# Performance work log

Measured on AMD Instinct MI355X. Metric: run time of the kernel, lower is better.

The kernel has to match this reference:

```python
import jax, jax.numpy as jnp
import numpy as np

B, L, D, H = 2, 4096, 512, 8
HD = D // H
SCALE = 1.0 / (D / H) ** 0.5


def setup_inputs() -> dict:
    key = jax.random.key(0)
    ks = jax.random.split(key, 12)
    s = 0.02
    inp = {
        "q": jax.random.normal(ks[0], (B, L, D), jnp.float32),
        "k": jax.random.normal(ks[1], (B, L, D), jnp.float32),
        "v": jax.random.normal(ks[2], (B, L, D), jnp.float32),
        # causal mask, True = keep (masked_fill where mask == False)
        "mask": jnp.tril(jnp.ones((L, L), bool))[None, None, :, :],
        "Wq": jax.random.normal(ks[3], (D, D), jnp.float32) * s,
        "bq": jnp.zeros((D,), jnp.float32),
        "Wk": jax.random.normal(ks[4], (D, D), jnp.float32) * s,
        "bk": jnp.zeros((D,), jnp.float32),
        "Wv": jax.random.normal(ks[5], (D, D), jnp.float32) * s,
        "bv": jnp.zeros((D,), jnp.float32),
        "Wo": jax.random.normal(ks[6], (D, D), jnp.float32) * s,
        "bo": jnp.zeros((D,), jnp.float32),
    }
    return inp


def _split_heads(x):
    # [B, L, D] -> [B, H, L, HD]
    b, l, d = x.shape
    return x.reshape(b, l, H, HD).transpose(0, 2, 1, 3)


def reference(q, k, v, mask, Wq, bq, Wk, bk, Wv, bv, Wo, bo):
    # Dropout is inference-mode (identity), matching module.eval().
    qh = _split_heads(q @ Wq.T + bq)          # [B,H,L,HD]
    kh = _split_heads(k @ Wk.T + bk)          # [B,H,L,HD]
    vh = _split_heads(v @ Wv.T + bv)          # [B,H,L,HD]
    scores = jnp.einsum("bhqd,bhkd->bhqk", qh, kh) * SCALE
    scores = jnp.where(mask, scores, -jnp.inf)
    attn = jax.nn.softmax(scores, axis=-1)
    out = jnp.einsum("bhqk,bhkd->bhqd", attn, vh)  # [B,H,L,HD]
    out = out.transpose(0, 2, 1, 3).reshape(q.shape[0], q.shape[1], D)
    return out @ Wo.T + bo
```

## Files before the change

### kernel.cpp

```cpp
#include <hip/hip_runtime.h>

typedef __bf16 bf16;
typedef __bf16 bf16x4 __attribute__((ext_vector_type(4)));
typedef __bf16 bf16x8 __attribute__((ext_vector_type(8)));
typedef float  f32x4  __attribute__((ext_vector_type(4)));
typedef float  f32x16 __attribute__((ext_vector_type(16)));
typedef unsigned int u32x2 __attribute__((ext_vector_type(2)));
typedef unsigned int u32x4 __attribute__((ext_vector_type(4)));

#define NB   2
#define NL   4096
#define ND   512
#define NH   8
#define NHD  64

static __device__ __forceinline__ void g2l16(const bf16* g, bf16* l) {
    __builtin_amdgcn_global_load_lds(
        (const __attribute__((address_space(1))) unsigned int*)g,
        (__attribute__((address_space(3))) unsigned int*)l, 16, 0, 0);
}

__global__ __launch_bounds__(256) void cvt_all(
    const float* __restrict__ q, const float* __restrict__ k, const float* __restrict__ v,
    const float* __restrict__ Wq, const float* __restrict__ Wk,
    const float* __restrict__ Wv, const float* __restrict__ Wo,
    bf16* __restrict__ qb, bf16* __restrict__ kb, bf16* __restrict__ vb,
    bf16* __restrict__ wqb, bf16* __restrict__ wkb,
    bf16* __restrict__ wvb, bf16* __restrict__ wob)
{
    const int z = blockIdx.z;
    const float* src; bf16* dst; int n4;
    switch (z) {
        case 0: src = q;  dst = qb;  n4 = NB * NL * ND / 4; break;
        case 1: src = k;  dst = kb;  n4 = NB * NL * ND / 4; break;
        case 2: src = v;  dst = vb;  n4 = NB * NL * ND / 4; break;
        case 3: src = Wq; dst = wqb; n4 = ND * ND / 4; break;
        case 4: src = Wk; dst = wkb; n4 = ND * ND / 4; break;
        case 5: src = Wv; dst = wvb; n4 = ND * ND / 4; break;
        default: src = Wo; dst = wob; n4 = ND * ND / 4; break;
    }
    for (int i = blockIdx.x * 256 + threadIdx.x; i < n4; i += gridDim.x * 256) {
        const f32x4 a = *(const f32x4*)(src + (size_t)i * 4);
        bf16x4 o;
        #pragma unroll
        for (int j = 0; j < 4; ++j) o[j] = (bf16)a[j];
        *(bf16x4*)(dst + (size_t)i * 4) = o;
    }
}

__global__ __launch_bounds__(256) void proj_qkv(
    const bf16* __restrict__ qb, const bf16* __restrict__ kb, const bf16* __restrict__ vb,
    const bf16* __restrict__ wq, const bf16* __restrict__ wk, const bf16* __restrict__ wv,
    const float* __restrict__ biasq, const float* __restrict__ biask, const float* __restrict__ biasv,
    bf16* __restrict__ qh, bf16* __restrict__ kh, bf16* __restrict__ vt)
{
    const int z = blockIdx.z;
    const bf16* X     = (z == 0) ? qb : (z == 1) ? kb : vb;
    const bf16* W     = (z == 0) ? wq : (z == 1) ? wk : wv;
    const float* bias = (z == 0) ? biasq : (z == 1) ? biask : biasv;

    const int m0 = blockIdx.y * 128;
    const int n0 = blockIdx.x * 128;

    __shared__ bf16 As[2][128 * 32];
    __shared__ bf16 Bs[2][128 * 32];

    const int t    = threadIdx.x;
    const int lane = t & 63;
    const int wm   = (t >> 7) & 1;
    const int wn   = (t >> 6) & 1;
    const int quad = lane >> 4;
    const int l16  = lane & 15;

    auto stage = [&](int k0, int buf) {
        #pragma unroll
        for (int p = 0; p < 2; ++p) {
            const int id = p * 256 + t;
            const int r = id >> 2, s = id & 3;
            const int c = (s ^ (r & 3)) * 8;
            g2l16(X + (size_t)(m0 + r) * ND + k0 + c, As[buf] + id * 8);
            g2l16(W + (size_t)(n0 + r) * ND + k0 + c, Bs[buf] + id * 8);
        }
    };

    f32x4 acc[4][4] = {};
    stage(0, 0);

    for (int it = 0; it < 16; ++it) {
        __syncthreads();
        if (it + 1 < 16) stage((it + 1) * 32, (it + 1) & 1);

        const bf16* as = As[it & 1];
        const bf16* bs = Bs[it & 1];
        bf16x8 aF[4], bF[4];
        #pragma unroll
        for (int i = 0; i < 4; ++i) {
            const int ra = wm * 64 + i * 16 + l16;
            const int rb = wn * 64 + i * 16 + l16;
            aF[i] = *(const bf16x8*)(as + ra * 32 + (quad ^ (ra & 3)) * 8);
            bF[i] = *(const bf16x8*)(bs + rb * 32 + (quad ^ (rb & 3)) * 8);
        }
        #pragma unroll
        for (int mt = 0; mt < 4; ++mt)
            #pragma unroll
            for (int nt = 0; nt < 4; ++nt)
                acc[mt][nt] = __builtin_amdgcn_mfma_f32_16x16x32_bf16(
                    aF[mt], bF[nt], acc[mt][nt], 0, 0, 0);
    }

    const float oscale = (z == 0) ? 0.125f : (z == 1) ? 1.4426950408889634f : 1.0f;
    #pragma unroll
    for (int nt = 0; nt < 4; ++nt) {
        const int col = n0 + wn * 64 + nt * 16 + l16;
        const float bb = bias[col];
        const int h = col >> 6, hd = col & 63;
        #pragma unroll
        for (int mt = 0; mt < 4; ++mt) {
            const int row0 = m0 + wm * 64 + mt * 16 + quad * 4;
            const int b = row0 >> 12;
            const int l = row0 & 4095;
            if (z == 2) {
                bf16x4 val;
                #pragma unroll
                for (int r = 0; r < 4; ++r) val[r] = (bf16)(acc[mt][nt][r] + bb);
                *(bf16x4*)(vt + ((size_t)(b * NH + h) * NHD + hd) * NL + l) = val;
            } else {
                bf16* dst = (z == 0) ? qh : kh;
                #pragma unroll
                for (int r = 0; r < 4; ++r)
                    dst[((size_t)(b * NH + h) * NL + (l + r)) * NHD + hd] =
                        (bf16)((acc[mt][nt][r] + bb) * oscale);
            }
        }
    }
}

__global__ __launch_bounds__(512, 2) void attn(
    const bf16* __restrict__ qh, const bf16* __restrict__ kh,
    const bf16* __restrict__ vt, bf16* __restrict__ ao)
{
    const int bh  = blockIdx.x;
    const int b   = bh >> 3, h = bh & 7;
    const int qtA = blockIdx.y;
    const int qtB = 31 - qtA;
    const int nAp = qtA + 1;

    __shared__ bf16 smem[65536];

    const int t    = threadIdx.x;
    const int wave = t >> 6;
    const int g    = wave >> 2;
    const int w4   = wave & 3;
    const int lane = t & 63;
    const int l32  = lane & 31;
    const int half = lane >> 5;
    const int sb   = g * 32768;
    const int tg   = t & 255;

    const bf16* Qg = qh + (size_t)bh * NL * NHD;
    const bf16* Kg = kh + (size_t)bh * NL * NHD;
    const bf16* Vg = vt + (size_t)bh * NHD * NL;

    #pragma unroll
    for (int p = 0; p < 4; ++p) {
        const int id = p * 512 + t;
        const int tile = id >> 10, r = (id >> 3) & 127, s = id & 7;
        const int q0 = (tile ? qtB : qtA) * 128;
        g2l16(Qg + (size_t)(q0 + r) * NHD + s * 8, smem + id * 8);
    }
    __syncthreads();

    bf16x8 qf[4];
    {
        const int qoff = (g == 0) ? 8192 : 0;
        #pragma unroll
        for (int c = 0; c < 4; ++c)
            qf[c] = *(const bf16x8*)(smem + qoff + (w4 * 32 + l32) * 64 + c * 16 + half * 8);
    }
    __syncthreads();

    auto stage_kv = [&](int k0, int buf) {
        bf16* kd = smem + sb + buf * 16384;
        bf16* vd = kd + 8192;
        #pragma unroll
        for (int p = 0; p < 4; ++p) {
            const int id = p * 256 + tg;
            const int r = id >> 3, s = id & 7;
            g2l16(Kg + (size_t)(k0 + r) * NHD + ((s ^ (r & 7)) * 8), kd + id * 8);
            const int ks2 = id >> 9, idh = id & 511;
            const int r2 = idh >> 3, s2 = idh & 7;
            g2l16(Vg + (size_t)r2 * NL + k0 + ks2 * 64 + ((s2 ^ (r2 & 7)) * 8),
                  vd + id * 8);
        }
    };

    stage_kv(((g == 0) ? (15 - qtA) : 0) * 128, 0);

    f32x16 o_acc[2] = {};
    float l_lane = 0.f;

    for (int jj = 0; jj < 17; ++jj) {
        __syncthreads();

        if (jj + 1 < 17) {
            const int jn = jj + 1;
            if (g == 0)          stage_kv((15 - qtA + jn) * 128, jn & 1);
            else if (jn < 16)    stage_kv(((jn < nAp) ? jn : jn - nAp) * 128, jn & 1);
        }

        if (g == 1 && jj == nAp) {
            const float lt = l_lane + __shfl_xor(l_lane, 32, 64);
            const float rcp = 1.0f / fmaxf(lt, 1e-20f);
            const int row = qtA * 128 + w4 * 32 + l32;
            #pragma unroll
            for (int mt2 = 0; mt2 < 2; ++mt2)
                #pragma unroll
                for (int rr = 0; rr < 4; ++rr) {
                    const int hd = mt2 * 32 + rr * 8 + half * 4;
                    bf16x4 val;
                    #pragma unroll
                    for (int rb = 0; rb < 4; ++rb)
                        val[rb] = (bf16)(o_acc[mt2][rr * 4 + rb] * rcp);
                    *(bf16x4*)(ao + ((size_t)b * NL + row) * ND + h * NHD + hd) = val;
                }
            o_acc[0] = (f32x16)(0.f); o_acc[1] = (f32x16)(0.f);
            l_lane = 0.f;
            const bf16* Qt = Qg + (size_t)(qtB * 128 + w4 * 32 + l32) * NHD;
            #pragma unroll
            for (int c = 0; c < 4; ++c)
                qf[c] = *(const bf16x8*)(Qt + c * 16 + half * 8);
        }

        const bool act = (g == 0) || (jj < 16);
        if (act) {
            const bool onA   = (g == 1) && (jj < nAp);
            const int tile   = (g == 0) ? (15 - qtA + jj) : (onA ? jj : jj - nAp);
            const int qt_cur = onA ? qtA : qtB;
            const bf16* kb_ = smem + sb + (jj & 1) * 16384;
            const bf16* vb_ = kb_ + 8192;
            const int qrow_l = w4 * 32 + l32;

            #pragma unroll
            for (int ksub = 0; ksub < 2; ++ksub) {
                const bf16* ks_ = kb_ + ksub * 4096;
                const bf16* vs_ = vb_ + ksub * 4096;
                const int j64 = tile * 2 + ksub;

                f32x16 sacc[2] = {};
                #pragma unroll
                for (int c = 0; c < 4; ++c) {
                    #pragma unroll
                    for (int mt = 0; mt < 2; ++mt) {
                        const int row   = mt * 32 + l32;
                        const int chunk = 2 * c + half;
                        const bf16x8 kf = *(const bf16x8*)(ks_ + row * 64 + ((chunk ^ (row & 7)) * 8));
                        sacc[mt] = __builtin_amdgcn_mfma_f32_32x32x16_bf16(
                            kf, qf[c], sacc[mt], 0, 0, 0);
                    }
                }

                const bool diag = (j64 >= 2 * qt_cur);
                const int  dq   = j64 * 64 - qt_cur * 128;
                #pragma unroll
                for (int mt = 0; mt < 2; ++mt) {
                    #pragma unroll
                    for (int r = 0; r < 16; ++r) {
                        const int kv = mt * 32 + (r & 3) + 8 * (r >> 2) + 4 * half;
                        float e;
                        if (diag && (dq + kv > qrow_l)) e = 0.f;
                        else e = __builtin_amdgcn_exp2f(sacc[mt][r]);
                        l_lane += e;
                        sacc[mt][r] = e;
                    }
                }

                #pragma unroll
                for (int c = 0; c < 4; ++c) {
                    const int mt = c >> 1;
                    const int b0 = (c & 1) * 8;
                    unsigned w0, w1, w2, w3;
                    asm("v_cvt_pk_bf16_f32 %0, %1, %2" : "=v"(w0)
                        : "v"(sacc[mt][b0 + 0]), "v"(sacc[mt][b0 + 1]));
                    asm("v_cvt_pk_bf16_f32 %0, %1, %2" : "=v"(w1)
                        : "v"(sacc[mt][b0 + 2]), "v"(sacc[mt][b0 + 3]));
                    asm("v_cvt_pk_bf16_f32 %0, %1, %2" : "=v"(w2)
                        : "v"(sacc[mt][b0 + 4]), "v"(sacc[mt][b0 + 5]));
                    asm("v_cvt_pk_bf16_f32 %0, %1, %2" : "=v"(w3)
                        : "v"(sacc[mt][b0 + 6]), "v"(sacc[mt][b0 + 7]));
                    const u32x2 s02 = __builtin_amdgcn_permlane32_swap(w0, w2, false, false);
                    const u32x2 s13 = __builtin_amdgcn_permlane32_swap(w1, w3, false, false);
                    u32x4 pw_ = { s02.x, s13.x, s02.y, s13.y };
                    bf16x8 pf;
                    __builtin_memcpy(&pf, &pw_, 16);
                    #pragma unroll
                    for (int mt2 = 0; mt2 < 2; ++mt2) {
                        const int row = mt2 * 32 + l32;
                        const int u8  = 2 * c + half;
                        const bf16x8 vf = *(const bf16x8*)(vs_ + row * 64 + ((u8 ^ (row & 7)) * 8));
                        o_acc[mt2] = __builtin_amdgcn_mfma_f32_32x32x16_bf16(
                            vf, pf, o_acc[mt2], 0, 0, 0);
                    }
                }
            }
        }
    }

    __syncthreads();
    float* comb = (float*)smem;
    if (g == 1) {
        const int base = w4 * (64 * 36) + lane * 36;
        #pragma unroll
        for (int mt2 = 0; mt2 < 2; ++mt2)
            #pragma unroll
            for (int i = 0; i < 16; ++i)
                comb[base + mt2 * 16 + i] = o_acc[mt2][i];
        const float lt = l_lane + __shfl_xor(l_lane, 32, 64);
        if (half == 0) comb[9216 + w4 * 32 + l32] = lt;
    }
    __syncthreads();
    if (g == 0) {
        const int base = w4 * (64 * 36) + lane * 36;
        const float lt = l_lane + __shfl_xor(l_lane, 32, 64)
                       + comb[9216 + w4 * 32 + l32];
        const float rcp = 1.0f / fmaxf(lt, 1e-20f);
        const int row = qtB * 128 + w4 * 32 + l32;
        #pragma unroll
        for (int mt2 = 0; mt2 < 2; ++mt2)
            #pragma unroll
            for (int rr = 0; rr < 4; ++rr) {
                const int hd = mt2 * 32 + rr * 8 + half * 4;
                bf16x4 val;
                #pragma unroll
                for (int rb = 0; rb < 4; ++rb)
                    val[rb] = (bf16)((o_acc[mt2][rr * 4 + rb] +
                                      comb[base + mt2 * 16 + rr * 4 + rb]) * rcp);
                *(bf16x4*)(ao + ((size_t)b * NL + row) * ND + h * NHD + hd) = val;
            }
    }
}

__global__ __launch_bounds__(256) void out_proj(
    const bf16* __restrict__ ao, const bf16* __restrict__ wo,
    const float* __restrict__ bo, float* __restrict__ out)
{
    const int m0 = blockIdx.y * 128;
    const int n0 = blockIdx.x * 128;

    __shared__ bf16 As[2][128 * 32];
    __shared__ bf16 Bs[2][128 * 32];

    const int t    = threadIdx.x;
    const int lane = t & 63;
    const int wm   = (t >> 7) & 1;
    const int wn   = (t >> 6) & 1;
    const int quad = lane >> 4;
    const int l16  = lane & 15;

    auto stage = [&](int k0, int buf) {
        #pragma unroll
        for (int p = 0; p < 2; ++p) {
            const int id = p * 256 + t;
            const int r = id >> 2, s = id & 3;
            const int c = (s ^ (r & 3)) * 8;
            g2l16(ao + (size_t)(m0 + r) * ND + k0 + c, As[buf] + id * 8);
            g2l16(wo + (size_t)(n0 + r) * ND + k0 + c, Bs[buf] + id * 8);
        }
    };

    f32x4 acc[4][4] = {};
    stage(0, 0);

    for (int it = 0; it < 16; ++it) {
        __syncthreads();
        if (it + 1 < 16) stage((it + 1) * 32, (it + 1) & 1);

        const bf16* as = As[it & 1];
        const bf16* bs = Bs[it & 1];
        bf16x8 aF[4], bF[4];
        #pragma unroll
        for (int i = 0; i < 4; ++i) {
            const int ra = wm * 64 + i * 16 + l16;
            const int rb = wn * 64 + i * 16 + l16;
            aF[i] = *(const bf16x8*)(as + ra * 32 + (quad ^ (ra & 3)) * 8);
            bF[i] = *(const bf16x8*)(bs + rb * 32 + (quad ^ (rb & 3)) * 8);
        }
        #pragma unroll
        for (int mt = 0; mt < 4; ++mt)
            #pragma unroll
            for (int nt = 0; nt < 4; ++nt)
                acc[mt][nt] = __builtin_amdgcn_mfma_f32_16x16x32_bf16(
                    aF[mt], bF[nt], acc[mt][nt], 0, 0, 0);
    }

    #pragma unroll
    for (int nt = 0; nt < 4; ++nt) {
        const int col = n0 + wn * 64 + nt * 16 + l16;
        const float bb = bo[col];
        #pragma unroll
        for (int mt = 0; mt < 4; ++mt) {
            const int row0 = m0 + wm * 64 + mt * 16 + quad * 4;
            #pragma unroll
            for (int r = 0; r < 4; ++r)
                out[(size_t)(row0 + r) * ND + col] = acc[mt][nt][r] + bb;
        }
    }
}

extern "C" void kernel_launch(void* const* d_in, const int* in_sizes, int n_in,
                              void* d_out, int out_size, void* d_ws, size_t ws_size,
                              hipStream_t stream) {
    (void)in_sizes; (void)n_in; (void)out_size; (void)ws_size;

    const float* q  = (const float*)d_in[0];
    const float* k  = (const float*)d_in[1];
    const float* v  = (const float*)d_in[2];
    const float* Wq = (const float*)d_in[4];
    const float* bq = (const float*)d_in[5];
    const float* Wk = (const float*)d_in[6];
    const float* bk = (const float*)d_in[7];
    const float* Wv = (const float*)d_in[8];
    const float* bv = (const float*)d_in[9];
    const float* Wo = (const float*)d_in[10];
    const float* bo = (const float*)d_in[11];

    const size_t XSZ = (size_t)NB * NL * ND;
    const size_t WSZ = (size_t)ND * ND;
    bf16* p = (bf16*)d_ws;
    bf16* qb  = p; p += XSZ;
    bf16* kb  = p; p += XSZ;
    bf16* vb  = p; p += XSZ;
    bf16* wqb = p; p += WSZ;
    bf16* wkb = p; p += WSZ;
    bf16* wvb = p; p += WSZ;
    bf16* wob = p; p += WSZ;
    bf16* qh  = p; p += XSZ;
    bf16* kh  = p; p += XSZ;
    bf16* vt  = p; p += XSZ;
    bf16* ao  = p; p += XSZ;

    cvt_all<<<dim3(512, 1, 7), 256, 0, stream>>>(
        q, k, v, Wq, Wk, Wv, Wo, qb, kb, vb, wqb, wkb, wvb, wob);

    dim3 g1(ND / 128, (NB * NL) / 128, 3);
    proj_qkv<<<g1, 256, 0, stream>>>(qb, kb, vb, wqb, wkb, wvb, bq, bk, bv, qh, kh, vt);

    dim3 g2(16, 16, 1);
    attn<<<g2, 512, 0, stream>>>(qh, kh, vt, ao);

    dim3 g3(ND / 128, (NB * NL) / 128, 1);
    out_proj<<<g3, 256, 0, stream>>>(ao, wob, bo, (float*)d_out);
}
```

Baseline: 239.8 us.

## Split attention wave-groups into separate blocks with atomic-counter partial combine

Each 512-thread attention block, previously two 4-wave groups sharing LDS and combining results through shared memory, becomes two 256-thread blocks along a new grid z dimension. Each block stages its own K/V tiles into half the LDS. When a query tile's work is split across both blocks, partial outputs and row sums go to global scratch (reusing the qb buffer). An atomic counter, zeroed in the conversion kernel, lets the second block to finish combine both halves and write the result. The goal is finer scheduling granularity and more resident blocks per CU, at the cost of extra global traffic, fences and atomics for the merge.

Measured after the change: 335.8 us. +40.0%, slower.

```diff
diff --git a/kernel.cpp b/kernel.cpp
--- a/kernel.cpp
+++ b/kernel.cpp
@@ -26,9 +26,11 @@
     const float* __restrict__ Wv, const float* __restrict__ Wo,
     bf16* __restrict__ qb, bf16* __restrict__ kb, bf16* __restrict__ vb,
     bf16* __restrict__ wqb, bf16* __restrict__ wkb,
-    bf16* __restrict__ wvb, bf16* __restrict__ wob)
+    bf16* __restrict__ wvb, bf16* __restrict__ wob,
+    unsigned* __restrict__ ctr)
 {
     const int z = blockIdx.z;
+    if (z == 0 && blockIdx.x == 0 && threadIdx.x < 256) ctr[threadIdx.x] = 0;
     const float* src; bf16* dst; int n4;
     switch (z) {
         case 0: src = q;  dst = qb;  n4 = NB * NL * ND / 4; break;
@@ -135,56 +137,45 @@
     }
 }
 
-__global__ __launch_bounds__(512, 2) void attn(
+__global__ __launch_bounds__(256, 2) void attn(
     const bf16* __restrict__ qh, const bf16* __restrict__ kh,
-    const bf16* __restrict__ vt, bf16* __restrict__ ao)
+    const bf16* __restrict__ vt, bf16* __restrict__ ao,
+    float* __restrict__ pO, float* __restrict__ pL, unsigned* __restrict__ ctr)
 {
     const int bh  = blockIdx.x;
     const int b   = bh >> 3, h = bh & 7;
     const int qtA = blockIdx.y;
+    const int z   = blockIdx.z;
     const int qtB = 31 - qtA;
     const int nAp = qtA + 1;
-
-    __shared__ bf16 smem[65536];
+    const int nB1 = 15 - qtA;
+    const int slot = bh * 16 + qtA;
+
+    __shared__ bf16 smem[32768];
+    __shared__ unsigned sflag;
 
     const int t    = threadIdx.x;
-    const int wave = t >> 6;
-    const int g    = wave >> 2;
-    const int w4   = wave & 3;
+    const int w4   = t >> 6;
     const int lane = t & 63;
     const int l32  = lane & 31;
     const int half = lane >> 5;
-    const int sb   = g * 32768;
-    const int tg   = t & 255;
+    const int qrow_l = w4 * 32 + l32;
 
     const bf16* Qg = qh + (size_t)bh * NL * NHD;
     const bf16* Kg = kh + (size_t)bh * NL * NHD;
     const bf16* Vg = vt + (size_t)bh * NHD * NL;
 
-    #pragma unroll
-    for (int p = 0; p < 4; ++p) {
-        const int id = p * 512 + t;
-        const int tile = id >> 10, r = (id >> 3) & 127, s = id & 7;
-        const int q0 = (tile ? qtB : qtA) * 128;
-        g2l16(Qg + (size_t)(q0 + r) * NHD + s * 8, smem + id * 8);
-    }
-    __syncthreads();
-
-    bf16x8 qf[4];
-    {
-        const int qoff = (g == 0) ? 8192 : 0;
-        #pragma unroll
-        for (int c = 0; c < 4; ++c)
-            qf[c] = *(const bf16x8*)(smem + qoff + (w4 * 32 + l32) * 64 + c * 16 + half * 8);
-    }
-    __syncthreads();
+    const int nT = (z == 0) ? 17 : 16;
+    auto tile_of = [&](int jj) -> int {
+        return (z == 0) ? (15 - qtA + jj) : ((jj < nAp) ? jj : jj - nAp);
+    };
 
     auto stage_kv = [&](int k0, int buf) {
-        bf16* kd = smem + sb + buf * 16384;
+        bf16* kd = smem + buf * 16384;
         bf16* vd = kd + 8192;
         #pragma unroll
         for (int p = 0; p < 4; ++p) {
-            const int id = p * 256 + tg;
+            const int id = p * 256 + t;
             const int r = id >> 3, s = id & 7;
             g2l16(Kg + (size_t)(k0 + r) * NHD + ((s ^ (r & 7)) * 8), kd + id * 8);
             const int ks2 = id >> 9, idh = id & 511;
@@ -194,136 +185,22 @@
         }
     };
 
-    stage_kv(((g == 0) ? (15 - qtA) : 0) * 128, 0);
+    stage_kv(tile_of(0) * 128, 0);
+
+    bf16x8 qf[4];
+    {
+        const int qt0 = (z == 0) ? qtB : qtA;
+        const bf16* Qt = Qg + (size_t)(qt0 * 128 + qrow_l) * NHD;
+        #pragma unroll
+        for (int c = 0; c < 4; ++c)
+            qf[c] = *(const bf16x8*)(Qt + c * 16 + half * 8);
+    }
 
     f32x16 o_acc[2] = {};
     float l_lane = 0.f;
 
-    for (int jj = 0; jj < 17; ++jj) {
-        __syncthreads();
-
-        if (jj + 1 < 17) {
-            const int jn = jj + 1;
-            if (g == 0)          stage_kv((15 - qtA + jn) * 128, jn & 1);
-            else if (jn < 16)    stage_kv(((jn < nAp) ? jn : jn - nAp) * 128, jn & 1);
-        }
-
-        if (g == 1 && jj == nAp) {
-            const float lt = l_lane + __shfl_xor(l_lane, 32, 64);
-            const float rcp = 1.0f / fmaxf(lt, 1e-20f);
-            const int row = qtA * 128 + w4 * 32 + l32;
-            #pragma unroll
-            for (int mt2 = 0; mt2 < 2; ++mt2)
-                #pragma unroll
-                for (int rr = 0; rr < 4; ++rr) {
-                    const int hd = mt2 * 32 + rr * 8 + half * 4;
-                    bf16x4 val;
-                    #pragma unroll
-                    for (int rb = 0; rb < 4; ++rb)
-                        val[rb] = (bf16)(o_acc[mt2][rr * 4 + rb] * rcp);
-                    *(bf16x4*)(ao + ((size_t)b * NL + row) * ND + h * NHD + hd) = val;
-                }
-            o_acc[0] = (f32x16)(0.f); o_acc[1] = (f32x16)(0.f);
-            l_lane = 0.f;
-            const bf16* Qt = Qg + (size_t)(qtB * 128 + w4 * 32 + l32) * NHD;
-            #pragma unroll
-            for (int c = 0; c < 4; ++c)
-                qf[c] = *(const bf16x8*)(Qt + c * 16 + half * 8);
-        }
-
-        const bool act = (g == 0) || (jj < 16);
-        if (act) {
-            const bool onA   = (g == 1) && (jj < nAp);
-            const int tile   = (g == 0) ? (15 - qtA + jj) : (onA ? jj : jj - nAp);
-            const int qt_cur = onA ? qtA : qtB;
-            const bf16* kb_ = smem + sb + (jj & 1) * 16384;
-            const bf16* vb_ = kb_ + 8192;
-            const int qrow_l = w4 * 32 + l32;
-
-            #pragma unroll
-            for (int ksub = 0; ksub < 2; ++ksub) {
-                const bf16* ks_ = kb_ + ksub * 4096;
-                const bf16* vs_ = vb_ + ksub * 4096;
-                const int j64 = tile * 2 + ksub;
-
-                f32x16 sacc[2] = {};
-                #pragma unroll
-                for (int c = 0; c < 4; ++c) {
-                    #pragma unroll
-                    for (int mt = 0; mt < 2; ++mt) {
-                        const int row   = mt * 32 + l32;
-                        const int chunk = 2 * c + half;
-                        const bf16x8 kf = *(const bf16x8*)(ks_ + row * 64 + ((chunk ^ (row & 7)) * 8));
-                        sacc[mt] = __builtin_amdgcn_mfma_f32_32x32x16_bf16(
-                            kf, qf[c], sacc[mt], 0, 0, 0);
-                    }
-                }
-
-                const bool diag = (j64 >= 2 * qt_cur);
-                const int  dq   = j64 * 64 - qt_cur * 128;
-                #pragma unroll
-                for (int mt = 0; mt < 2; ++mt) {
-                    #pragma unroll
-                    for (int r = 0; r < 16; ++r) {
-                        const int kv = mt * 32 + (r & 3) + 8 * (r >> 2) + 4 * half;
-                        float e;
-                        if (diag && (dq + kv > qrow_l)) e = 0.f;
-                        else e = __builtin_amdgcn_exp2f(sacc[mt][r]);
-                        l_lane += e;
-                        sacc[mt][r] = e;
-                    }
-                }
-
-                #pragma unroll
-                for (int c = 0; c < 4; ++c) {
-                    const int mt = c >> 1;
-                    const int b0 = (c & 1) * 8;
-                    unsigned w0, w1, w2, w3;
-                    asm("v_cvt_pk_bf16_f32 %0, %1, %2" : "=v"(w0)
-                        : "v"(sacc[mt][b0 + 0]), "v"(sacc[mt][b0 + 1]));
-                    asm("v_cvt_pk_bf16_f32 %0, %1, %2" : "=v"(w1)
-                        : "v"(sacc[mt][b0 + 2]), "v"(sacc[mt][b0 + 3]));
-                    asm("v_cvt_pk_bf16_f32 %0, %1, %2" : "=v"(w2)
-                        : "v"(sacc[mt][b0 + 4]), "v"(sacc[mt][b0 + 5]));
-                    asm("v_cvt_pk_bf16_f32 %0, %1, %2" : "=v"(w3)
-                        : "v"(sacc[mt][b0 + 6]), "v"(sacc[mt][b0 + 7]));
-                    const u32x2 s02 = __builtin_amdgcn_permlane32_swap(w0, w2, false, false);
-                    const u32x2 s13 = __builtin_amdgcn_permlane32_swap(w1, w3, false, false);
-                    u32x4 pw_ = { s02.x, s13.x, s02.y, s13.y };
-                    bf16x8 pf;
-                    __builtin_memcpy(&pf, &pw_, 16);
-                    #pragma unroll
-                    for (int mt2 = 0; mt2 < 2; ++mt2) {
-                        const int row = mt2 * 32 + l32;
-                        const int u8  = 2 * c + half;
-                        const bf16x8 vf = *(const bf16x8*)(vs_ + row * 64 + ((u8 ^ (row & 7)) * 8));
-                        o_acc[mt2] = __builtin_amdgcn_mfma_f32_32x32x16_bf16(
-                            vf, pf, o_acc[mt2], 0, 0, 0);
-                    }
-                }
-            }
-        }
-    }
-
-    __syncthreads();
-    float* comb = (float*)smem;
-    if (g == 1) {
-        const int base = w4 * (64 * 36) + lane * 36;
-        #pragma unroll
-        for (int mt2 = 0; mt2 < 2; ++mt2)
-            #pragma unroll
-            for (int i = 0; i < 16; ++i)
-                comb[base + mt2 * 16 + i] = o_acc[mt2][i];
-        const float lt = l_lane + __shfl_xor(l_lane, 32, 64);
-        if (half == 0) comb[9216 + w4 * 32 + l32] = lt;
-    }
-    __syncthreads();
-    if (g == 0) {
-        const int base = w4 * (64 * 36) + lane * 36;
-        const float lt = l_lane + __shfl_xor(l_lane, 32, 64)
-                       + comb[9216 + w4 * 32 + l32];
-        const float rcp = 1.0f / fmaxf(lt, 1e-20f);
-        const int row = qtB * 128 + w4 * 32 + l32;
+    auto write_out = [&](int qt, float rcp) {
+        const int row = qt * 128 + qrow_l;
         #pragma unroll
         for (int mt2 = 0; mt2 < 2; ++mt2)
             #pragma unroll
@@ -332,8 +209,141 @@
                 bf16x4 val;
                 #pragma unroll
                 for (int rb = 0; rb < 4; ++rb)
-                    val[rb] = (bf16)((o_acc[mt2][rr * 4 + rb] +
-                                      comb[base + mt2 * 16 + rr * 4 + rb]) * rcp);
+                    val[rb] = (bf16)(o_acc[mt2][rr * 4 + rb] * rcp);
+                *(bf16x4*)(ao + ((size_t)b * NL + row) * ND + h * NHD + hd) = val;
+            }
+    };
+
+    for (int jj = 0; jj < nT; ++jj) {
+        __syncthreads();
+
+        if (jj + 1 < nT) stage_kv(tile_of(jj + 1) * 128, (jj + 1) & 1);
+
+        if (z == 1 && jj == nAp) {
+            const float lt = l_lane + __shfl_xor(l_lane, 32, 64);
+            write_out(qtA, 1.0f / fmaxf(lt, 1e-20f));
+            o_acc[0] = (f32x16)(0.f); o_acc[1] = (f32x16)(0.f);
+            l_lane = 0.f;
+            const bf16* Qt = Qg + (size_t)(qtB * 128 + qrow_l) * NHD;
+            #pragma unroll
+            for (int c = 0; c < 4; ++c)
+                qf[c] = *(const bf16x8*)(Qt + c * 16 + half * 8);
+        }
+
+        const int tile   = tile_of(jj);
+        const int qt_cur = (z == 0) ? qtB : ((jj < nAp) ? qtA : qtB);
+        const bf16* kb_ = smem + (jj & 1) * 16384;
+        const bf16* vb_ = kb_ + 8192;
+
+        #pragma unroll
+        for (int ksub = 0; ksub < 2; ++ksub) {
+            const bf16* ks_ = kb_ + ksub * 4096;
+            const bf16* vs_ = vb_ + ksub * 4096;
+            const int j64 = tile * 2 + ksub;
+
+            f32x16 sacc[2] = {};
+            #pragma unroll
+            for (int c = 0; c < 4; ++c) {
+                #pragma unroll
+                for (int mt = 0; mt < 2; ++mt) {
+                    const int row   = mt * 32 + l32;
+                    const int chunk = 2 * c + half;
+                    const bf16x8 kf = *(const bf16x8*)(ks_ + row * 64 + ((chunk ^ (row & 7)) * 8));
+                    sacc[mt] = __builtin_amdgcn_mfma_f32_32x32x16_bf16(
+                        kf, qf[c], sacc[mt], 0, 0, 0);
+                }
+            }
+
+            const bool diag = (j64 >= 2 * qt_cur);
+            const int  dq   = j64 * 64 - qt_cur * 128;
+            #pragma unroll
+            for (int mt = 0; mt < 2; ++mt) {
+                #pragma unroll
+                for (int r = 0; r < 16; ++r) {
+                    const int kv = mt * 32 + (r & 3) + 8 * (r >> 2) + 4 * half;
+                    float e;
+                    if (diag && (dq + kv > qrow_l)) e = 0.f;
+                    else e = __builtin_amdgcn_exp2f(sacc[mt][r]);
+                    l_lane += e;
+                    sacc[mt][r] = e;
+                }
+            }
+
+            #pragma unroll
+            for (int c = 0; c < 4; ++c) {
+                const int mt = c >> 1;
+                const int b0 = (c & 1) * 8;
+                unsigned w0, w1, w2, w3;
+                asm("v_cvt_pk_bf16_f32 %0, %1, %2" : "=v"(w0)
+                    : "v"(sacc[mt][b0 + 0]), "v"(sacc[mt][b0 + 1]));
+                asm("v_cvt_pk_bf16_f32 %0, %1, %2" : "=v"(w1)
+                    : "v"(sacc[mt][b0 + 2]), "v"(sacc[mt][b0 + 3]));
+                asm("v_cvt_pk_bf16_f32 %0, %1, %2" : "=v"(w2)
+                    : "v"(sacc[mt][b0 + 4]), "v"(sacc[mt][b0 + 5]));
+                asm("v_cvt_pk_bf16_f32 %0, %1, %2" : "=v"(w3)
+                    : "v"(sacc[mt][b0 + 6]), "v"(sacc[mt][b0 + 7]));
+                const u32x2 s02 = __builtin_amdgcn_permlane32_swap(w0, w2, false, false);
+                const u32x2 s13 = __builtin_amdgcn_permlane32_swap(w1, w3, false, false);
+                u32x4 pw_ = { s02.x, s13.x, s02.y, s13.y };
+                bf16x8 pf;
+                __builtin_memcpy(&pf, &pw_, 16);
+                #pragma unroll
+                for (int mt2 = 0; mt2 < 2; ++mt2) {
+                    const int row = mt2 * 32 + l32;
+                    const int u8  = 2 * c + half;
+                    const bf16x8 vf = *(const bf16x8*)(vs_ + row * 64 + ((u8 ^ (row & 7)) * 8));
+                    o_acc[mt2] = __builtin_amdgcn_mfma_f32_32x32x16_bf16(
+                        vf, pf, o_acc[mt2], 0, 0, 0);
+                }
+            }
+        }
+    }
+
+    if (z == 1 && nAp == 16) {
+        const float lt = l_lane + __shfl_xor(l_lane, 32, 64);
+        write_out(qtA, 1.0f / fmaxf(lt, 1e-20f));
+        return;
+    }
+
+    const float lt = l_lane + __shfl_xor(l_lane, 32, 64);
+
+    if (z == 0 && nB1 == 0) {
+        write_out(qtB, 1.0f / fmaxf(lt, 1e-20f));
+        return;
+    }
+
+    float* myO = pO + ((size_t)slot * 2 + z) * 8192;
+    #pragma unroll
+    for (int mt2 = 0; mt2 < 2; ++mt2)
+        #pragma unroll
+        for (int rr = 0; rr < 4; ++rr) {
+            f32x4 v4;
+            #pragma unroll
+            for (int rb = 0; rb < 4; ++rb) v4[rb] = o_acc[mt2][rr * 4 + rb];
+            *(f32x4*)(myO + qrow_l * 64 + mt2 * 32 + rr * 8 + half * 4) = v4;
+        }
+    if (half == 0) pL[(slot * 2 + z) * 128 + qrow_l] = lt;
+
+    __threadfence();
+    __syncthreads();
+    if (t == 0) sflag = atomicAdd(ctr + slot, 1u);
+    __syncthreads();
+    if (sflag == 1) {
+        __threadfence();
+        const float* oO = pO + ((size_t)slot * 2 + (1 - z)) * 8192;
+        const float lo  = pL[(slot * 2 + (1 - z)) * 128 + qrow_l];
+        const float rcp = 1.0f / fmaxf(lt + lo, 1e-20f);
+        const int row = qtB * 128 + qrow_l;
+        #pragma unroll
+        for (int mt2 = 0; mt2 < 2; ++mt2)
+            #pragma unroll
+            for (int rr = 0; rr < 4; ++rr) {
+                const int hd = mt2 * 32 + rr * 8 + half * 4;
+                const f32x4 ov = *(const f32x4*)(oO + qrow_l * 64 + hd);
+                bf16x4 val;
+                #pragma unroll
+                for (int rb = 0; rb < 4; ++rb)
+                    val[rb] = (bf16)((o_acc[mt2][rr * 4 + rb] + ov[rb]) * rcp);
                 *(bf16x4*)(ao + ((size_t)b * NL + row) * ND + h * NHD + hd) = val;
             }
     }
@@ -437,15 +447,19 @@
     bf16* kh  = p; p += XSZ;
     bf16* vt  = p; p += XSZ;
     bf16* ao  = p; p += XSZ;
+    unsigned* ctr = (unsigned*)p;
+
+    float* pO = (float*)qb;
+    float* pL = pO + (size_t)256 * 2 * 8192;
 
     cvt_all<<<dim3(512, 1, 7), 256, 0, stream>>>(
-        q, k, v, Wq, Wk, Wv, Wo, qb, kb, vb, wqb, wkb, wvb, wob);
+        q, k, v, Wq, Wk, Wv, Wo, qb, kb, vb, wqb, wkb, wvb, wob, ctr);
 
     dim3 g1(ND / 128, (NB * NL) / 128, 3);
     proj_qkv<<<g1, 256, 0, stream>>>(qb, kb, vb, wqb, wkb, wvb, bq, bk, bv, qh, kh, vt);
 
-    dim3 g2(16, 16, 1);
-    attn<<<g2, 512, 0, stream>>>(qh, kh, vt, ao);
+    dim3 g2(16, 16, 2);
+    attn<<<g2, 256, 0, stream>>>(qh, kh, vt, ao, pO, pL, ctr);
 
     dim3 g3(ND / 128, (NB * NL) / 128, 1);
     out_proj<<<g3, 256, 0, stream>>>(ao, wob, bo, (float*)d_out);
```

## Widen K tile to 128 and stage GEMM epilogues through LDS for coalesced stores

Applied to the files above, without the earlier changes.

Both projection GEMMs now load 128-wide K slices (4 iterations instead of 16) into a 128KB LDS double buffer with an 8-way XOR swizzle, cutting barrier and loop overhead. Their epilogues first write results to padded LDS tiles, then emit 16-byte coalesced global stores (including the transposed V layout) instead of scattered 2-byte or 4-byte stores. The cost is a 1-block-per-CU occupancy limit from the large LDS footprint and an extra LDS round trip in the epilogue.

Measured after the change: 242.8 us. No clear change (+1.2%).

```diff
diff --git a/kernel.cpp b/kernel.cpp
--- a/kernel.cpp
+++ b/kernel.cpp
@@ -48,7 +48,7 @@
     }
 }
 
-__global__ __launch_bounds__(256) void proj_qkv(
+__global__ __launch_bounds__(256, 1) void proj_qkv(
     const bf16* __restrict__ qb, const bf16* __restrict__ kb, const bf16* __restrict__ vb,
     const bf16* __restrict__ wq, const bf16* __restrict__ wk, const bf16* __restrict__ wv,
     const float* __restrict__ biasq, const float* __restrict__ biask, const float* __restrict__ biasv,
@@ -62,8 +62,7 @@
     const int m0 = blockIdx.y * 128;
     const int n0 = blockIdx.x * 128;
 
-    __shared__ bf16 As[2][128 * 32];
-    __shared__ bf16 Bs[2][128 * 32];
+    __shared__ bf16 smem[65536];
 
     const int t    = threadIdx.x;
     const int lane = t & 63;
@@ -74,63 +73,94 @@
 
     auto stage = [&](int k0, int buf) {
         #pragma unroll
-        for (int p = 0; p < 2; ++p) {
+        for (int p = 0; p < 8; ++p) {
             const int id = p * 256 + t;
-            const int r = id >> 2, s = id & 3;
-            const int c = (s ^ (r & 3)) * 8;
-            g2l16(X + (size_t)(m0 + r) * ND + k0 + c, As[buf] + id * 8);
-            g2l16(W + (size_t)(n0 + r) * ND + k0 + c, Bs[buf] + id * 8);
+            const int r = id >> 4, s = id & 15;
+            const int c = (s ^ (r & 7)) * 8;
+            g2l16(X + (size_t)(m0 + r) * ND + k0 + c, smem + buf * 16384 + id * 8);
+            g2l16(W + (size_t)(n0 + r) * ND + k0 + c, smem + 32768 + buf * 16384 + id * 8);
         }
     };
 
     f32x4 acc[4][4] = {};
     stage(0, 0);
 
-    for (int it = 0; it < 16; ++it) {
+    for (int it = 0; it < 4; ++it) {
         __syncthreads();
-        if (it + 1 < 16) stage((it + 1) * 32, (it + 1) & 1);
-
-        const bf16* as = As[it & 1];
-        const bf16* bs = Bs[it & 1];
-        bf16x8 aF[4], bF[4];
-        #pragma unroll
-        for (int i = 0; i < 4; ++i) {
-            const int ra = wm * 64 + i * 16 + l16;
-            const int rb = wn * 64 + i * 16 + l16;
-            aF[i] = *(const bf16x8*)(as + ra * 32 + (quad ^ (ra & 3)) * 8);
-            bF[i] = *(const bf16x8*)(bs + rb * 32 + (quad ^ (rb & 3)) * 8);
-        }
-        #pragma unroll
-        for (int mt = 0; mt < 4; ++mt)
-            #pragma unroll
-            for (int nt = 0; nt < 4; ++nt)
-                acc[mt][nt] = __builtin_amdgcn_mfma_f32_16x16x32_bf16(
-                    aF[mt], bF[nt], acc[mt][nt], 0, 0, 0);
-    }
-
+        if (it + 1 < 4) stage((it + 1) * 128, (it + 1) & 1);
+
+        const bf16* as = smem + (it & 1) * 16384;
+        const bf16* bs = smem + 32768 + (it & 1) * 16384;
+        #pragma unroll
+        for (int kk = 0; kk < 4; ++kk) {
+            bf16x8 aF[4], bF[4];
+            #pragma unroll
+            for (int i = 0; i < 4; ++i) {
+                const int ra = wm * 64 + i * 16 + l16;
+                const int rb = wn * 64 + i * 16 + l16;
+                aF[i] = *(const bf16x8*)(as + ra * 128 + (((kk * 4 + quad) ^ (ra & 7)) * 8));
+                bF[i] = *(const bf16x8*)(bs + rb * 128 + (((kk * 4 + quad) ^ (rb & 7)) * 8));
+            }
+            #pragma unroll
+            for (int mt = 0; mt < 4; ++mt)
+                #pragma unroll
+                for (int nt = 0; nt < 4; ++nt)
+                    acc[mt][nt] = __builtin_amdgcn_mfma_f32_16x16x32_bf16(
+                        aF[mt], bF[nt], acc[mt][nt], 0, 0, 0);
+        }
+    }
+
+    __syncthreads();
     const float oscale = (z == 0) ? 0.125f : (z == 1) ? 1.4426950408889634f : 1.0f;
-    #pragma unroll
-    for (int nt = 0; nt < 4; ++nt) {
-        const int col = n0 + wn * 64 + nt * 16 + l16;
-        const float bb = bias[col];
-        const int h = col >> 6, hd = col & 63;
-        #pragma unroll
-        for (int mt = 0; mt < 4; ++mt) {
-            const int row0 = m0 + wm * 64 + mt * 16 + quad * 4;
-            const int b = row0 >> 12;
-            const int l = row0 & 4095;
-            if (z == 2) {
-                bf16x4 val;
-                #pragma unroll
-                for (int r = 0; r < 4; ++r) val[r] = (bf16)(acc[mt][nt][r] + bb);
-                *(bf16x4*)(vt + ((size_t)(b * NH + h) * NHD + hd) * NL + l) = val;
-            } else {
-                bf16* dst = (z == 0) ? qh : kh;
-                #pragma unroll
-                for (int r = 0; r < 4; ++r)
-                    dst[((size_t)(b * NH + h) * NL + (l + r)) * NHD + hd] =
-                        (bf16)((acc[mt][nt][r] + bb) * oscale);
-            }
+    const int b = m0 >> 12;
+    const int l0 = m0 & 4095;
+    bf16* Cs = smem;
+
+    if (z == 2) {
+        #pragma unroll
+        for (int nt = 0; nt < 4; ++nt) {
+            const int col = wn * 64 + nt * 16 + l16;
+            const float bb = bias[n0 + col];
+            #pragma unroll
+            for (int mt = 0; mt < 4; ++mt) {
+                const int rowm = wm * 64 + mt * 16 + quad * 4;
+                #pragma unroll
+                for (int rb = 0; rb < 4; ++rb)
+                    Cs[col * 136 + rowm + rb] = (bf16)(acc[mt][nt][rb] + bb);
+            }
+        }
+        __syncthreads();
+        #pragma unroll
+        for (int p = 0; p < 8; ++p) {
+            const int id = p * 256 + t;
+            const int c = id >> 4, kc = id & 15;
+            const int gcol = n0 + c;
+            const int h = gcol >> 6, hd = gcol & 63;
+            const bf16x8 v8 = *(const bf16x8*)(Cs + c * 136 + kc * 8);
+            *(bf16x8*)(vt + ((size_t)(b * NH + h) * NHD + hd) * NL + l0 + kc * 8) = v8;
+        }
+    } else {
+        #pragma unroll
+        for (int nt = 0; nt < 4; ++nt) {
+            const int col = wn * 64 + nt * 16 + l16;
+            const float bb = bias[n0 + col];
+            #pragma unroll
+            for (int mt = 0; mt < 4; ++mt) {
+                const int rowm = wm * 64 + mt * 16 + quad * 4;
+                #pragma unroll
+                for (int rb = 0; rb < 4; ++rb)
+                    Cs[(rowm + rb) * 136 + col] = (bf16)((acc[mt][nt][rb] + bb) * oscale);
+            }
+        }
+        __syncthreads();
+        bf16* dst = (z == 0) ? qh : kh;
+        const int h0 = n0 >> 6;
+        #pragma unroll
+        for (int p = 0; p < 8; ++p) {
+            const int id = p * 256 + t;
+            const int r = id >> 4, j = (id >> 3) & 1, kc = id & 7;
+            const bf16x8 v8 = *(const bf16x8*)(Cs + r * 136 + j * 64 + kc * 8);
+            *(bf16x8*)(dst + ((size_t)(b * NH + h0 + j) * NL + l0 + r) * NHD + kc * 8) = v8;
         }
     }
 }
@@ -339,15 +369,14 @@
     }
 }
 
-__global__ __launch_bounds__(256) void out_proj(
+__global__ __launch_bounds__(256, 1) void out_proj(
     const bf16* __restrict__ ao, const bf16* __restrict__ wo,
     const float* __restrict__ bo, float* __restrict__ out)
 {
     const int m0 = blockIdx.y * 128;
     const int n0 = blockIdx.x * 128;
 
-    __shared__ bf16 As[2][128 * 32];
-    __shared__ bf16 Bs[2][128 * 32];
+    __shared__ bf16 smem[65536];
 
     const int t    = threadIdx.x;
     const int lane = t & 63;
@@ -358,51 +387,64 @@
 
     auto stage = [&](int k0, int buf) {
         #pragma unroll
-        for (int p = 0; p < 2; ++p) {
+        for (int p = 0; p < 8; ++p) {
             const int id = p * 256 + t;
-            const int r = id >> 2, s = id & 3;
-            const int c = (s ^ (r & 3)) * 8;
-            g2l16(ao + (size_t)(m0 + r) * ND + k0 + c, As[buf] + id * 8);
-            g2l16(wo + (size_t)(n0 + r) * ND + k0 + c, Bs[buf] + id * 8);
+            const int r = id >> 4, s = id & 15;
+            const int c = (s ^ (r & 7)) * 8;
+            g2l16(ao + (size_t)(m0 + r) * ND + k0 + c, smem + buf * 16384 + id * 8);
+            g2l16(wo + (size_t)(n0 + r) * ND + k0 + c, smem + 32768 + buf * 16384 + id * 8);
         }
     };
 
     f32x4 acc[4][4] = {};
     stage(0, 0);
 
-    for (int it = 0; it < 16; ++it) {
+    for (int it = 0; it < 4; ++it) {
         __syncthreads();
-        if (it + 1 < 16) stage((it + 1) * 32, (it + 1) & 1);
-
-        const bf16* as = As[it & 1];
-        const bf16* bs = Bs[it & 1];
-        bf16x8 aF[4], bF[4];
-        #pragma unroll
-        for (int i = 0; i < 4; ++i) {
-            const int ra = wm * 64 + i * 16 + l16;
-            const int rb = wn * 64 + i * 16 + l16;
-            aF[i] = *(const bf16x8*)(as + ra * 32 + (quad ^ (ra & 3)) * 8);
-            bF[i] = *(const bf16x8*)(bs + rb * 32 + (quad ^ (rb & 3)) * 8);
-        }
-        #pragma unroll
-        for (int mt = 0; mt < 4; ++mt)
-            #pragma unroll
-            for (int nt = 0; nt < 4; ++nt)
-                acc[mt][nt] = __builtin_amdgcn_mfma_f32_16x16x32_bf16(
-                    aF[mt], bF[nt], acc[mt][nt], 0, 0, 0);
-    }
-
+        if (it + 1 < 4) stage((it + 1) * 128, (it + 1) & 1);
+
+        const bf16* as = smem + (it & 1) * 16384;
+        const bf16* bs = smem + 32768 + (it & 1) * 16384;
+        #pragma unroll
+        for (int kk = 0; kk < 4; ++kk) {
+            bf16x8 aF[4], bF[4];
+            #pragma unroll
+            for (int i = 0; i < 4; ++i) {
+                const int ra = wm * 64 + i * 16 + l16;
+                const int rb = wn * 64 + i * 16 + l16;
+                aF[i] = *(const bf16x8*)(as + ra * 128 + (((kk * 4 + quad) ^ (ra & 7)) * 8));
+                bF[i] = *(const bf16x8*)(bs + rb * 128 + (((kk * 4 + quad) ^ (rb & 7)) * 8));
+            }
+            #pragma unroll
+            for (int mt = 0; mt < 4; ++mt)
+                #pragma unroll
+                for (int nt = 0; nt < 4; ++nt)
+                    acc[mt][nt] = __builtin_amdgcn_mfma_f32_16x16x32_bf16(
+                        aF[mt], bF[nt], acc[mt][nt], 0, 0, 0);
+        }
+    }
+
+    __syncthreads();
+    float* Cs = (float*)smem;
     #pragma unroll
     for (int nt = 0; nt < 4; ++nt) {
-        const int col = n0 + wn * 64 + nt * 16 + l16;
-        const float bb = bo[col];
+        const int col = wn * 64 + nt * 16 + l16;
+        const float bb = bo[n0 + col];
         #pragma unroll
         for (int mt = 0; mt < 4; ++mt) {
-            const int row0 = m0 + wm * 64 + mt * 16 + quad * 4;
-            #pragma unroll
-            for (int r = 0; r < 4; ++r)
-                out[(size_t)(row0 + r) * ND + col] = acc[mt][nt][r] + bb;
-        }
+            const int rowm = wm * 64 + mt * 16 + quad * 4;
+            #pragma unroll
+            for (int rb = 0; rb < 4; ++rb)
+                Cs[(rowm + rb) * 132 + col] = acc[mt][nt][rb] + bb;
+        }
+    }
+    __syncthreads();
+    #pragma unroll
+    for (int p = 0; p < 16; ++p) {
+        const int id = p * 256 + t;
+        const int r = id >> 5, kc = id & 31;
+        const f32x4 v4 = *(const f32x4*)(Cs + r * 132 + kc * 4);
+        *(f32x4*)(out + (size_t)(m0 + r) * ND + n0 + kc * 4) = v4;
     }
 }
 
```
